# Optimization experiments

Measured on AMD Instinct MI355X. Metric: run time of the kernel, lower is better.

Reference implementation:

```python
import jax, jax.numpy as jnp
import numpy as np

N_NODES = 100000
N_EDGES = 1600000
IN_DIM, HID_DIM, OUT_DIM = 128, 64, 40


def setup_inputs() -> dict:
    key = jax.random.key(0)
    k = jax.random.split(key, 6)
    feats = jax.random.normal(k[0], (N_NODES, IN_DIM), dtype=jnp.float32)
    src = jax.random.randint(k[1], (N_EDGES,), 0, N_NODES)
    dst = jax.random.randint(k[2], (N_EDGES,), 0, N_NODES)
    # Glorot-ish init for the two GraphConv weights
    W1 = jax.random.normal(k[3], (IN_DIM, HID_DIM), dtype=jnp.float32) * (2.0 / (IN_DIM + HID_DIM)) ** 0.5
    b1 = jnp.zeros((HID_DIM,), dtype=jnp.float32)
    W2 = jax.random.normal(k[4], (HID_DIM, OUT_DIM), dtype=jnp.float32) * (2.0 / (HID_DIM + OUT_DIM)) ** 0.5
    b2 = jnp.zeros((OUT_DIM,), dtype=jnp.float32)
    return {"feats": feats, "W1": W1, "b1": b1, "W2": W2, "b2": b2, "src": src, "dst": dst}


def _graph_conv(h, W, b, src, dst, n):
    # DGL GraphConv, norm='both': out = D_dst^{-1/2} * A^T * (D_src^{-1/2} * h) W + b
    # (weight applied before aggregation since in_feats > out_feats for both layers)
    ones_e = jnp.ones(src.shape, dtype=h.dtype)
    deg_out = jax.ops.segment_sum(ones_e, src, num_segments=n)
    deg_in = jax.ops.segment_sum(ones_e, dst, num_segments=n)
    norm_src = jnp.clip(deg_out, 1.0) ** -0.5  # [N]
    norm_dst = jnp.clip(deg_in, 1.0) ** -0.5   # [N]
    h = h * norm_src[:, None]
    h = h @ W                                   # [N, out]
    m = jax.ops.segment_sum(h[src], dst, num_segments=n)  # gather-scatter over edges
    return m * norm_dst[:, None] + b


def reference(feats, W1, b1, W2, b2, src, dst):
    n = feats.shape[0]
    # layer 0: GraphConv with relu activation (dropout is identity in eval)
    h1 = jax.nn.relu(_graph_conv(feats, W1, b1, src, dst, n))
    # layer 1: GraphConv, no activation
    h2 = _graph_conv(h1, W2, b2, src, dst, n)
    # GCN.forward returns (h_list, h); h_list holds the hidden layer output
    return (h1, h2)
```

## Files before the change

### kernel.cpp

```cpp
#include <hip/hip_runtime.h>
#include <hip/hip_bf16.h>

constexpr int N_NODES = 100000;
constexpr int N_EDGES = 1600000;
constexpr int IN_DIM  = 128;
constexpr int HID_DIM = 64;
constexpr int OUT_DIM = 40;

constexpr int BK_SHIFT = 9;
constexpr int NBKT = (N_NODES + 511) >> 9;
constexpr int ECAP = 9216;
constexpr int TILE = 4096;
constexpr int EPT  = TILE / 256;
constexpr int NTILES = (N_EDGES + TILE - 1) / TILE;
constexpr int GEMM_BLK = (N_NODES + 63) / 64;

typedef __attribute__((ext_vector_type(8))) short short8;
typedef __attribute__((ext_vector_type(4))) float f32x4;

__device__ inline float bf2f(unsigned int u16) {
  union { float f; unsigned int i; } c;
  c.i = u16 << 16;
  return c.f;
}

__device__ inline unsigned short f2bf(float f) {
  union { float f; unsigned int u; } c; c.f = f;
  unsigned int u = c.u + 0x7fffu + ((c.u >> 16) & 1u);
  return (unsigned short)(u >> 16);
}

__global__ void k_init(const float* __restrict__ W1, const float* __restrict__ W2,
                       unsigned short* __restrict__ Bfrag1, unsigned short* __restrict__ Bfrag2,
                       int* __restrict__ gcur) {
  int tid = blockIdx.x * blockDim.x + threadIdx.x;
  int stride = gridDim.x * blockDim.x;
  for (int i = tid; i < 2 * NBKT; i += stride) gcur[i] = 0;
  for (int idx = tid; idx < 4 * 4 * 64 * 8; idx += stride) {
    int j = idx & 7;
    int lane = (idx >> 3) & 63;
    int nt = (idx >> 9) & 3;
    int ks = idx >> 11;
    int k = ks * 32 + 8 * (lane >> 4) + j;
    int col = nt * 16 + (lane & 15);
    Bfrag1[idx] = f2bf(W1[k * HID_DIM + col]);
  }
  for (int idx = tid; idx < 2 * 3 * 64 * 8; idx += stride) {
    int j = idx & 7;
    int lane = (idx >> 3) & 63;
    int nt = (idx >> 9) % 3;
    int ks = idx / (3 * 512);
    int k = ks * 32 + 8 * (lane >> 4) + j;
    int col = nt * 16 + (lane & 15);
    Bfrag2[idx] = (col < OUT_DIM) ? f2bf(W2[k * OUT_DIM + col]) : (unsigned short)0;
  }
}

__global__ __launch_bounds__(256) void k_part(const int* __restrict__ src,
                                              const int* __restrict__ dst,
                                              int* __restrict__ gcur,
                                              int* __restrict__ gcur2,
                                              unsigned int* __restrict__ pairs,
                                              unsigned short* __restrict__ spart) {
  __shared__ int scnt[NBKT], soff[NBKT], gbase[NBKT];
  __shared__ int scnt2[NBKT], soff2[NBKT], gbase2[NBKT];
  __shared__ int sc1[256], sc2[256];
  __shared__ unsigned int sord[TILE];
  __shared__ unsigned char sordB[TILE];
  __shared__ unsigned short sordS[TILE];
  __shared__ unsigned char sordSB[TILE];
  int tid = threadIdx.x;
  int tileBase = blockIdx.x * TILE;
  int tcnt = N_EDGES - tileBase; if (tcnt > TILE) tcnt = TILE;
  if (tid < NBKT) { scnt[tid] = 0; scnt2[tid] = 0; }
  __syncthreads();
  int s_[EPT], d_[EPT], pos_[EPT], pos2_[EPT];
#pragma unroll
  for (int t = 0; t < EPT; ++t) {
    int idx = tileBase + t * 256 + tid;
    if (idx < N_EDGES) {
      s_[t] = src[idx];
      d_[t] = dst[idx];
      pos_[t]  = atomicAdd(&scnt[d_[t] >> BK_SHIFT], 1);
      pos2_[t] = atomicAdd(&scnt2[s_[t] >> BK_SHIFT], 1);
    }
  }
  __syncthreads();
  int v1 = (tid < NBKT) ? scnt[tid] : 0;
  int v2 = (tid < NBKT) ? scnt2[tid] : 0;
  sc1[tid] = v1; sc2[tid] = v2;
  __syncthreads();
  for (int o = 1; o < 256; o <<= 1) {
    int x1 = (tid >= o) ? sc1[tid - o] : 0;
    int x2 = (tid >= o) ? sc2[tid - o] : 0;
    __syncthreads();
    sc1[tid] += x1; sc2[tid] += x2;
    __syncthreads();
  }
  if (tid < NBKT) {
    soff[tid]  = sc1[tid] - v1;
    soff2[tid] = sc2[tid] - v2;
    gbase[tid]  = v1 ? atomicAdd(&gcur[tid],  v1) : 0;
    gbase2[tid] = v2 ? atomicAdd(&gcur2[tid], v2) : 0;
  }
  __syncthreads();
#pragma unroll
  for (int t = 0; t < EPT; ++t) {
    int idx = tileBase + t * 256 + tid;
    if (idx < N_EDGES) {
      int b  = d_[t] >> BK_SHIFT;
      int b2 = s_[t] >> BK_SHIFT;
      int p  = soff[b] + pos_[t];
      int p2 = soff2[b2] + pos2_[t];
      sord[p]  = (unsigned)s_[t] | ((unsigned)(d_[t] & 511) << 17);
      sordB[p] = (unsigned char)b;
      sordS[p2]  = (unsigned short)(s_[t] & 511);
      sordSB[p2] = (unsigned char)b2;
    }
  }
  __syncthreads();
  for (int i = tid; i < tcnt; i += 256) {
    int b = sordB[i];
    int g = gbase[b] + (i - soff[b]);
    if (g < ECAP) pairs[(size_t)b * ECAP + g] = sord[i];
  }
  for (int i = tid; i < tcnt; i += 256) {
    int b = sordSB[i];
    int g = gbase2[b] + (i - soff2[b]);
    if (g < ECAP) spart[(size_t)b * ECAP + g] = sordS[i];
  }
}

__global__ __launch_bounds__(256) void k_csrdeg(const unsigned int* __restrict__ pairs,
                                                const unsigned short* __restrict__ spart,
                                                const int* __restrict__ gcur,
                                                const int* __restrict__ gcur2,
                                                int* __restrict__ startg,
                                                int* __restrict__ cntg,
                                                float* __restrict__ norm_dst,
                                                float* __restrict__ norm_src,
                                                int* __restrict__ esrc) {
  __shared__ int cnt[512];
  __shared__ int off[512];
  __shared__ int cur[512];
  __shared__ int wsum[256];
  __shared__ int esrcL[ECAP];
  int tid = threadIdx.x;
  if (blockIdx.x >= NBKT) {
    int b = blockIdx.x - NBKT;
    int node0 = b << BK_SHIFT;
    int nNodes = N_NODES - node0; if (nNodes > 512) nNodes = 512;
    int E = gcur2[b]; if (E > ECAP) E = ECAP;
    cnt[tid] = 0; cnt[tid + 256] = 0;
    __syncthreads();
    const unsigned short* sp = spart + (size_t)b * ECAP;
    for (int i = tid; i < E; i += 256) atomicAdd(&cnt[sp[i]], 1);
    __syncthreads();
    for (int j = tid; j < nNodes; j += 256) {
      int c = cnt[j];
      norm_src[node0 + j] = rsqrtf((float)(c < 1 ? 1 : c));
    }
    return;
  }
  int b = blockIdx.x;
  int node0 = b << BK_SHIFT;
  int nNodes = N_NODES - node0; if (nNodes > 512) nNodes = 512;
  int E = gcur[b]; if (E > ECAP) E = ECAP;
  cnt[tid] = 0; cnt[tid + 256] = 0;
  __syncthreads();
  const unsigned int* pp = pairs + (size_t)b * ECAP;
  for (int i = tid; i < E; i += 256) atomicAdd(&cnt[pp[i] >> 17], 1);
  __syncthreads();
  int v0 = cnt[tid * 2], v1 = cnt[tid * 2 + 1];
  int s = v0 + v1;
  wsum[tid] = s; __syncthreads();
  for (int o = 1; o < 256; o <<= 1) {
    int x = (tid >= o) ? wsum[tid - o] : 0;
    __syncthreads();
    wsum[tid] += x;
    __syncthreads();
  }
  int excl = wsum[tid] - s;
  off[tid * 2] = excl;     cur[tid * 2] = excl;
  off[tid * 2 + 1] = excl + v0; cur[tid * 2 + 1] = excl + v0;
  __syncthreads();
  for (int i = tid; i < E; i += 256) {
    unsigned p = pp[i];
    int pos = atomicAdd(&cur[p >> 17], 1);
    esrcL[pos] = (int)(p & 0x1FFFFu);
  }
  __syncthreads();
  int base = b * ECAP;
  for (int i = tid; i < E; i += 256) esrc[base + i] = esrcL[i];
  for (int j = tid; j < nNodes; j += 256) {
    int c = cnt[j];
    startg[node0 + j] = base + off[j];
    cntg[node0 + j] = c;
    norm_dst[node0 + j] = rsqrtf((float)(c < 1 ? 1 : c));
  }
}

__global__ __launch_bounds__(256) void k_gemm1_mfma(
    const float* __restrict__ feats, const uint4* __restrict__ Bfrag1,
    const float* __restrict__ norm_src, __hip_bfloat16* __restrict__ t1) {
  int tid = threadIdx.x;
  int w = tid >> 6, lane = tid & 63;
  int row0 = blockIdx.x * 64 + w * 16;
  int arow = row0 + (lane & 15);
  int arowc = arow < N_NODES ? arow : N_NODES - 1;
  int half = lane >> 4;

  const float4* fr = (const float4*)(feats + (size_t)arowc * IN_DIM);
  f32x4 acc[4] = {{0.f,0.f,0.f,0.f},{0.f,0.f,0.f,0.f},{0.f,0.f,0.f,0.f},{0.f,0.f,0.f,0.f}};
#pragma unroll
  for (int ks = 0; ks < 4; ++ks) {
    float4 p0 = fr[ks * 8 + 2 * half];
    float4 p1 = fr[ks * 8 + 2 * half + 1];
    short8 a;
    a[0] = (short)f2bf(p0.x); a[1] = (short)f2bf(p0.y);
    a[2] = (short)f2bf(p0.z); a[3] = (short)f2bf(p0.w);
    a[4] = (short)f2bf(p1.x); a[5] = (short)f2bf(p1.y);
    a[6] = (short)f2bf(p1.z); a[7] = (short)f2bf(p1.w);
#pragma unroll
    for (int nt = 0; nt < 4; ++nt) {
      uint4 bu = Bfrag1[(ks * 4 + nt) * 64 + lane];
      short8 b = *(const short8*)&bu;
      acc[nt] = __builtin_amdgcn_mfma_f32_16x16x32_bf16(a, b, acc[nt], 0, 0, 0);
    }
  }
  int col = lane & 15;
  int rbase = row0 + half * 4;
#pragma unroll
  for (int r = 0; r < 4; ++r) {
    int grow = rbase + r;
    if (grow < N_NODES) {
      float ns = norm_src[grow];
#pragma unroll
      for (int nt = 0; nt < 4; ++nt) {
        unsigned short h = f2bf(acc[nt][r] * ns);
        *((unsigned short*)t1 + (size_t)grow * HID_DIM + nt * 16 + col) = h;
      }
    }
  }
}

__global__ __launch_bounds__(256) void k_agg1g2(
    const uint4* __restrict__ t1, const int* __restrict__ startg,
    const int* __restrict__ cntg, const int* __restrict__ esrc,
    const float* __restrict__ norm_dst, const float* __restrict__ norm_src,
    const float4* __restrict__ b1v, const uint4* __restrict__ Bfrag2,
    float4* __restrict__ out1, __hip_bfloat16* __restrict__ t2) {
  __shared__ unsigned short h1s[32][64];
  int tid = threadIdx.x;
  int g = tid >> 3, q = tid & 7;
  int n = blockIdx.x * 32 + g;
  int s0 = startg[n];
  int c  = cntg[n];
  const int* bk = esrc + s0;
  float a0 = 0.f, a1 = 0.f, a2 = 0.f, a3 = 0.f;
  float a4 = 0.f, a5 = 0.f, a6 = 0.f, a7 = 0.f;
  for (int i = 0; i < c; i += 8) {
#pragma unroll
    for (int t = 0; t < 8; ++t) {
      int ii = i + t;
      bool ok = ii < c;
      int s = bk[ok ? ii : 0];
      uint4 v = t1[(size_t)s * 8 + q];
      unsigned vx = ok ? v.x : 0u;
      unsigned vy = ok ? v.y : 0u;
      unsigned vz = ok ? v.z : 0u;
      unsigned vw = ok ? v.w : 0u;
      a0 += bf2f(vx & 0xffffu); a1 += bf2f(vx >> 16);
      a2 += bf2f(vy & 0xffffu); a3 += bf2f(vy >> 16);
      a4 += bf2f(vz & 0xffffu); a5 += bf2f(vz >> 16);
      a6 += bf2f(vw & 0xffffu); a7 += bf2f(vw >> 16);
    }
  }
  float nd = norm_dst[n];
  float4 bb0 = b1v[q * 2];
  float4 bb1 = b1v[q * 2 + 1];
  float h0 = fmaxf(a0 * nd + bb0.x, 0.f);
  float h1 = fmaxf(a1 * nd + bb0.y, 0.f);
  float h2 = fmaxf(a2 * nd + bb0.z, 0.f);
  float h3 = fmaxf(a3 * nd + bb0.w, 0.f);
  float h4 = fmaxf(a4 * nd + bb1.x, 0.f);
  float h5 = fmaxf(a5 * nd + bb1.y, 0.f);
  float h6 = fmaxf(a6 * nd + bb1.z, 0.f);
  float h7 = fmaxf(a7 * nd + bb1.w, 0.f);
  out1[(size_t)n * 16 + q * 2]     = make_float4(h0, h1, h2, h3);
  out1[(size_t)n * 16 + q * 2 + 1] = make_float4(h4, h5, h6, h7);
  float ns = norm_src[n];
  uint4 pk;
  pk.x = (unsigned)f2bf(h0 * ns) | ((unsigned)f2bf(h1 * ns) << 16);
  pk.y = (unsigned)f2bf(h2 * ns) | ((unsigned)f2bf(h3 * ns) << 16);
  pk.z = (unsigned)f2bf(h4 * ns) | ((unsigned)f2bf(h5 * ns) << 16);
  pk.w = (unsigned)f2bf(h6 * ns) | ((unsigned)f2bf(h7 * ns) << 16);
  *(uint4*)&h1s[g][q * 8] = pk;
  __syncthreads();
  if (tid < 128) {
    int wave = tid >> 6;
    int lane = tid & 63;
    int r = lane & 15, half = lane >> 4;
    int row = wave * 16 + r;
    f32x4 acc[3] = {{0.f,0.f,0.f,0.f},{0.f,0.f,0.f,0.f},{0.f,0.f,0.f,0.f}};
#pragma unroll
    for (int ks = 0; ks < 2; ++ks) {
      short8 a = *(const short8*)&h1s[row][ks * 32 + 8 * half];
#pragma unroll
      for (int nt = 0; nt < 3; ++nt) {
        uint4 bu = Bfrag2[(ks * 3 + nt) * 64 + lane];
        short8 b = *(const short8*)&bu;
        acc[nt] = __builtin_amdgcn_mfma_f32_16x16x32_bf16(a, b, acc[nt], 0, 0, 0);
      }
    }
    int col = lane & 15;
#pragma unroll
    for (int r2 = 0; r2 < 4; ++r2) {
      int node = blockIdx.x * 32 + wave * 16 + half * 4 + r2;
#pragma unroll
      for (int nt = 0; nt < 3; ++nt) {
        int j = nt * 16 + col;
        if (j < OUT_DIM)
          *((unsigned short*)t2 + (size_t)node * OUT_DIM + j) = f2bf(acc[nt][r2]);
      }
    }
  }
}

__global__ __launch_bounds__(256) void k_agg2(
    const uint4* __restrict__ t2, const int* __restrict__ startg,
    const int* __restrict__ cntg, const int* __restrict__ esrc,
    const float* __restrict__ norm_dst, const float* __restrict__ b2,
    float4* __restrict__ out2) {
  int idx = blockIdx.x * blockDim.x + threadIdx.x;
  int n = idx / 5;
  int q = idx - n * 5;
  if (n >= N_NODES) return;
  int s0 = startg[n];
  int c  = cntg[n];
  const int* bk = esrc + s0;
  float a0 = 0.f, a1 = 0.f, a2 = 0.f, a3 = 0.f;
  float a4 = 0.f, a5 = 0.f, a6 = 0.f, a7 = 0.f;
  for (int i = 0; i < c; i += 8) {
#pragma unroll
    for (int t = 0; t < 8; ++t) {
      int ii = i + t;
      bool ok = ii < c;
      int s = bk[ok ? ii : 0];
      uint4 v = t2[(size_t)s * 5 + q];
      unsigned vx = ok ? v.x : 0u;
      unsigned vy = ok ? v.y : 0u;
      unsigned vz = ok ? v.z : 0u;
      unsigned vw = ok ? v.w : 0u;
      a0 += bf2f(vx & 0xffffu); a1 += bf2f(vx >> 16);
      a2 += bf2f(vy & 0xffffu); a3 += bf2f(vy >> 16);
      a4 += bf2f(vz & 0xffffu); a5 += bf2f(vz >> 16);
      a6 += bf2f(vw & 0xffffu); a7 += bf2f(vw >> 16);
    }
  }
  float nd = norm_dst[n];
  float4 bb0 = *(const float4*)(b2 + q * 8);
  float4 bb1 = *(const float4*)(b2 + q * 8 + 4);
  out2[(size_t)n * 10 + q * 2] =
      make_float4(a0 * nd + bb0.x, a1 * nd + bb0.y, a2 * nd + bb0.z, a3 * nd + bb0.w);
  out2[(size_t)n * 10 + q * 2 + 1] =
      make_float4(a4 * nd + bb1.x, a5 * nd + bb1.y, a6 * nd + bb1.z, a7 * nd + bb1.w);
}

extern "C" void kernel_launch(void* const* d_in, const int* in_sizes, int n_in,
                              void* d_out, int out_size, void* d_ws, size_t ws_size,
                              hipStream_t stream) {
  const float* feats = (const float*)d_in[0];
  const float* W1    = (const float*)d_in[1];
  const float* b1    = (const float*)d_in[2];
  const float* W2    = (const float*)d_in[3];
  const float* b2    = (const float*)d_in[4];
  const int*   src   = (const int*)d_in[5];
  const int*   dst   = (const int*)d_in[6];

  float* out  = (float*)d_out;
  float* out1 = out;
  float* out2 = out + (size_t)N_NODES * HID_DIM;

  __hip_bfloat16* t1 = (__hip_bfloat16*)d_ws;
  __hip_bfloat16* t2 = t1 + (size_t)N_NODES * HID_DIM;
  unsigned int* pairs = (unsigned int*)(t2 + (size_t)N_NODES * OUT_DIM);
  unsigned short* spart = (unsigned short*)(pairs + (size_t)NBKT * ECAP);
  int* esrc   = (int*)(spart + (size_t)NBKT * ECAP);
  unsigned short* Bfrag1 = (unsigned short*)(esrc + (size_t)NBKT * ECAP);
  unsigned short* Bfrag2 = Bfrag1 + 4 * 4 * 64 * 8;
  int* startg = (int*)(Bfrag2 + 2 * 3 * 64 * 8);
  int* cntg   = startg + N_NODES;
  float* norm_src = (float*)(cntg + N_NODES);
  float* norm_dst = norm_src + N_NODES;
  int* gcur  = (int*)(norm_dst + N_NODES);
  int* gcur2 = gcur + NBKT;

  k_init<<<16, 256, 0, stream>>>(W1, W2, Bfrag1, Bfrag2, gcur);
  k_part<<<NTILES, 256, 0, stream>>>(src, dst, gcur, gcur2, pairs, spart);
  k_csrdeg<<<2 * NBKT, 256, 0, stream>>>(pairs, spart, gcur, gcur2,
                                         startg, cntg, norm_dst, norm_src, esrc);

  k_gemm1_mfma<<<GEMM_BLK, 256, 0, stream>>>(feats, (const uint4*)Bfrag1, norm_src, t1);
  k_agg1g2<<<N_NODES / 32, 256, 0, stream>>>((const uint4*)t1, startg, cntg, esrc,
                                             norm_dst, norm_src, (const float4*)b1,
                                             (const uint4*)Bfrag2, (float4*)out1, t2);
  k_agg2<<<(N_NODES * 5 + 255) / 256, 256, 0, stream>>>((const uint4*)t2, startg, cntg, esrc,
                                                        norm_dst, b2, (float4*)out2);
}
```

Baseline: 133.8 us.

## Merge CSR/degree build with layer-1 GEMM and defer source norm to aggregation

Folds the layer-1 MFMA GEMM into the CSR/degree kernel as extra blocks, so the GEMM no longer waits on norm_src and one launch is removed. The source-degree normalization is moved from the GEMM epilogue into the aggregation loop, where each edge gathers norm_src[s] and scales the features by it. This lets the memory-bound GEMM overlap with the histogram and scan blocks. The cost is an extra scattered scalar load plus multiplies per edge in the aggregation. The GEMM blocks also share the large LDS footprint of the CSR path, which may limit occupancy.

```diff
diff --git a/kernel.cpp b/kernel.cpp
--- a/kernel.cpp
+++ b/kernel.cpp
@@ -131,23 +131,69 @@
   }
 }
 
-__global__ __launch_bounds__(256) void k_csrdeg(const unsigned int* __restrict__ pairs,
-                                                const unsigned short* __restrict__ spart,
-                                                const int* __restrict__ gcur,
-                                                const int* __restrict__ gcur2,
-                                                int* __restrict__ startg,
-                                                int* __restrict__ cntg,
-                                                float* __restrict__ norm_dst,
-                                                float* __restrict__ norm_src,
-                                                int* __restrict__ esrc) {
+__global__ __launch_bounds__(256) void k_mid(const unsigned int* __restrict__ pairs,
+                                             const unsigned short* __restrict__ spart,
+                                             const int* __restrict__ gcur,
+                                             const int* __restrict__ gcur2,
+                                             int* __restrict__ startg,
+                                             int* __restrict__ cntg,
+                                             float* __restrict__ norm_dst,
+                                             float* __restrict__ norm_src,
+                                             int* __restrict__ esrc,
+                                             const float* __restrict__ feats,
+                                             const uint4* __restrict__ Bfrag1,
+                                             __hip_bfloat16* __restrict__ t1) {
   __shared__ int cnt[512];
   __shared__ int off[512];
   __shared__ int cur[512];
   __shared__ int wsum[256];
   __shared__ int esrcL[ECAP];
   int tid = threadIdx.x;
-  if (blockIdx.x >= NBKT) {
-    int b = blockIdx.x - NBKT;
+  int bx = blockIdx.x;
+
+  if (bx >= 2 * NBKT) {
+    int blk = bx - 2 * NBKT;
+    int w = tid >> 6, lane = tid & 63;
+    int row0 = blk * 64 + w * 16;
+    int arow = row0 + (lane & 15);
+    int arowc = arow < N_NODES ? arow : N_NODES - 1;
+    int half = lane >> 4;
+    const float4* fr = (const float4*)(feats + (size_t)arowc * IN_DIM);
+    f32x4 acc[4] = {{0.f,0.f,0.f,0.f},{0.f,0.f,0.f,0.f},{0.f,0.f,0.f,0.f},{0.f,0.f,0.f,0.f}};
+#pragma unroll
+    for (int ks = 0; ks < 4; ++ks) {
+      float4 p0 = fr[ks * 8 + 2 * half];
+      float4 p1 = fr[ks * 8 + 2 * half + 1];
+      short8 a;
+      a[0] = (short)f2bf(p0.x); a[1] = (short)f2bf(p0.y);
+      a[2] = (short)f2bf(p0.z); a[3] = (short)f2bf(p0.w);
+      a[4] = (short)f2bf(p1.x); a[5] = (short)f2bf(p1.y);
+      a[6] = (short)f2bf(p1.z); a[7] = (short)f2bf(p1.w);
+#pragma unroll
+      for (int nt = 0; nt < 4; ++nt) {
+        uint4 bu = Bfrag1[(ks * 4 + nt) * 64 + lane];
+        short8 b = *(const short8*)&bu;
+        acc[nt] = __builtin_amdgcn_mfma_f32_16x16x32_bf16(a, b, acc[nt], 0, 0, 0);
+      }
+    }
+    int col = lane & 15;
+    int rbase = row0 + half * 4;
+#pragma unroll
+    for (int r = 0; r < 4; ++r) {
+      int grow = rbase + r;
+      if (grow < N_NODES) {
+#pragma unroll
+        for (int nt = 0; nt < 4; ++nt) {
+          unsigned short h = f2bf(acc[nt][r]);
+          *((unsigned short*)t1 + (size_t)grow * HID_DIM + nt * 16 + col) = h;
+        }
+      }
+    }
+    return;
+  }
+
+  if (bx >= NBKT) {
+    int b = bx - NBKT;
     int node0 = b << BK_SHIFT;
     int nNodes = N_NODES - node0; if (nNodes > 512) nNodes = 512;
     int E = gcur2[b]; if (E > ECAP) E = ECAP;
@@ -162,7 +208,8 @@
     }
     return;
   }
-  int b = blockIdx.x;
+
+  int b = bx;
   int node0 = b << BK_SHIFT;
   int nNodes = N_NODES - node0; if (nNodes > 512) nNodes = 512;
   int E = gcur[b]; if (E > ECAP) E = ECAP;
@@ -197,50 +244,6 @@
     startg[node0 + j] = base + off[j];
     cntg[node0 + j] = c;
     norm_dst[node0 + j] = rsqrtf((float)(c < 1 ? 1 : c));
-  }
-}
-
-__global__ __launch_bounds__(256) void k_gemm1_mfma(
-    const float* __restrict__ feats, const uint4* __restrict__ Bfrag1,
-    const float* __restrict__ norm_src, __hip_bfloat16* __restrict__ t1) {
-  int tid = threadIdx.x;
-  int w = tid >> 6, lane = tid & 63;
-  int row0 = blockIdx.x * 64 + w * 16;
-  int arow = row0 + (lane & 15);
-  int arowc = arow < N_NODES ? arow : N_NODES - 1;
-  int half = lane >> 4;
-
-  const float4* fr = (const float4*)(feats + (size_t)arowc * IN_DIM);
-  f32x4 acc[4] = {{0.f,0.f,0.f,0.f},{0.f,0.f,0.f,0.f},{0.f,0.f,0.f,0.f},{0.f,0.f,0.f,0.f}};
-#pragma unroll
-  for (int ks = 0; ks < 4; ++ks) {
-    float4 p0 = fr[ks * 8 + 2 * half];
-    float4 p1 = fr[ks * 8 + 2 * half + 1];
-    short8 a;
-    a[0] = (short)f2bf(p0.x); a[1] = (short)f2bf(p0.y);
-    a[2] = (short)f2bf(p0.z); a[3] = (short)f2bf(p0.w);
-    a[4] = (short)f2bf(p1.x); a[5] = (short)f2bf(p1.y);
-    a[6] = (short)f2bf(p1.z); a[7] = (short)f2bf(p1.w);
-#pragma unroll
-    for (int nt = 0; nt < 4; ++nt) {
-      uint4 bu = Bfrag1[(ks * 4 + nt) * 64 + lane];
-      short8 b = *(const short8*)&bu;
-      acc[nt] = __builtin_amdgcn_mfma_f32_16x16x32_bf16(a, b, acc[nt], 0, 0, 0);
-    }
-  }
-  int col = lane & 15;
-  int rbase = row0 + half * 4;
-#pragma unroll
-  for (int r = 0; r < 4; ++r) {
-    int grow = rbase + r;
-    if (grow < N_NODES) {
-      float ns = norm_src[grow];
-#pragma unroll
-      for (int nt = 0; nt < 4; ++nt) {
-        unsigned short h = f2bf(acc[nt][r] * ns);
-        *((unsigned short*)t1 + (size_t)grow * HID_DIM + nt * 16 + col) = h;
-      }
-    }
   }
 }
 
@@ -265,15 +268,12 @@
       int ii = i + t;
       bool ok = ii < c;
       int s = bk[ok ? ii : 0];
+      float nss = ok ? norm_src[s] : 0.f;
       uint4 v = t1[(size_t)s * 8 + q];
-      unsigned vx = ok ? v.x : 0u;
-      unsigned vy = ok ? v.y : 0u;
-      unsigned vz = ok ? v.z : 0u;
-      unsigned vw = ok ? v.w : 0u;
-      a0 += bf2f(vx & 0xffffu); a1 += bf2f(vx >> 16);
-      a2 += bf2f(vy & 0xffffu); a3 += bf2f(vy >> 16);
-      a4 += bf2f(vz & 0xffffu); a5 += bf2f(vz >> 16);
-      a6 += bf2f(vw & 0xffffu); a7 += bf2f(vw >> 16);
+      a0 += nss * bf2f(v.x & 0xffffu); a1 += nss * bf2f(v.x >> 16);
+      a2 += nss * bf2f(v.y & 0xffffu); a3 += nss * bf2f(v.y >> 16);
+      a4 += nss * bf2f(v.z & 0xffffu); a5 += nss * bf2f(v.z >> 16);
+      a6 += nss * bf2f(v.w & 0xffffu); a7 += nss * bf2f(v.w >> 16);
     }
   }
   float nd = norm_dst[n];
@@ -398,10 +398,9 @@
 
   k_init<<<16, 256, 0, stream>>>(W1, W2, Bfrag1, Bfrag2, gcur);
   k_part<<<NTILES, 256, 0, stream>>>(src, dst, gcur, gcur2, pairs, spart);
-  k_csrdeg<<<2 * NBKT, 256, 0, stream>>>(pairs, spart, gcur, gcur2,
-                                         startg, cntg, norm_dst, norm_src, esrc);
-
-  k_gemm1_mfma<<<GEMM_BLK, 256, 0, stream>>>(feats, (const uint4*)Bfrag1, norm_src, t1);
+  k_mid<<<2 * NBKT + GEMM_BLK, 256, 0, stream>>>(pairs, spart, gcur, gcur2,
+                                                 startg, cntg, norm_dst, norm_src, esrc,
+                                                 feats, (const uint4*)Bfrag1, t1);
   k_agg1g2<<<N_NODES / 32, 256, 0, stream>>>((const uint4*)t1, startg, cntg, esrc,
                                              norm_dst, norm_src, (const float4*)b1,
                                              (const uint4*)Bfrag2, (float4*)out1, t2);
```

Measured after the change: 142.9 us. 1.07x slower.
